# Optimization experiments

Hardware: AMD Instinct MI355X
Metric: run time of the kernel (lower is better)

Reference implementation:

```python
import jax, jax.numpy as jnp
import numpy as np

FILTER_LENGTH = 1024
HOP_LENGTH = 512
CUTOFF = FILTER_LENGTH // 2 + 1  # 513
PAD = FILTER_LENGTH // 2


def _make_forward_basis():
    # Real/imag DFT basis, rows = [Re(0..cutoff-1); Im(0..cutoff-1)], cols = time taps
    fb = np.fft.fft(np.eye(FILTER_LENGTH))
    basis = np.vstack([np.real(fb[:CUTOFF, :]), np.imag(fb[:CUTOFF, :])]).astype(np.float32)
    # periodic ('fftbins') Hann window, win_length == filter_length so no centering pad
    n = np.arange(FILTER_LENGTH)
    window = (0.5 - 0.5 * np.cos(2.0 * np.pi * n / FILTER_LENGTH)).astype(np.float32)
    return jnp.asarray(basis * window[None, :])  # [1026, 1024]


def setup_inputs() -> dict:
    key = jax.random.key(0)
    input_data = jax.random.normal(key, (16, 1048576), dtype=jnp.float32)
    forward_basis = _make_forward_basis()
    return {"input_data": input_data, "forward_basis": forward_basis}


def reference(input_data, forward_basis):
    # reflect-pad, frame, windowed DFT via conv1d, then magnitude
    x = jnp.pad(input_data, ((0, 0), (PAD, PAD)), mode="reflect")[:, None, :]  # [B,1,L+1024]
    y = jax.lax.conv_general_dilated(
        x,
        forward_basis[:, None, :],  # [1026, 1, 1024]
        window_strides=(HOP_LENGTH,),
        padding="VALID",
        dimension_numbers=("NCH", "OIH", "NCH"),
    )  # [B, 1026, T]
    real = y[:, :CUTOFF, :]
    imag = y[:, CUTOFF:, :]
    return jnp.sqrt(real * real + imag * imag)  # [B, 513, T]
```

## Files before the change

### kernel.cpp

```cpp
#include <hip/hip_runtime.h>
#include <math.h>

#define L_IN   1048576
#define NBATCH 16
#define T_FR   2049
#define NBINS  513

struct C2 { float r, i; };
__device__ __forceinline__ C2 cadd(C2 a, C2 b){ return {a.r+b.r, a.i+b.i}; }
__device__ __forceinline__ C2 csub(C2 a, C2 b){ return {a.r-b.r, a.i-b.i}; }
__device__ __forceinline__ C2 cmul(C2 a, C2 b){ return {a.r*b.r - a.i*b.i, a.r*b.i + a.i*b.r}; }
__device__ __forceinline__ C2 cnegi(C2 a){ return {a.i, -a.r}; }
#define RSQ2 0.70710678118654752f
__device__ __forceinline__ C2 cw8 (C2 a){ return { RSQ2*(a.r+a.i),  RSQ2*(a.i-a.r)}; }
__device__ __forceinline__ C2 cw83(C2 a){ return { RSQ2*(a.i-a.r), -RSQ2*(a.r+a.i)}; }

__device__ __forceinline__ void dft8(const C2 x[8], C2 y[8]) {
  C2 ea0 = cadd(x[0], x[4]), ea1 = csub(x[0], x[4]);
  C2 eb0 = cadd(x[2], x[6]), eb1 = csub(x[2], x[6]);
  C2 oa0 = cadd(x[1], x[5]), oa1 = csub(x[1], x[5]);
  C2 ob0 = cadd(x[3], x[7]), ob1 = csub(x[3], x[7]);
  C2 E0 = cadd(ea0, eb0), E2 = csub(ea0, eb0);
  C2 nb = cnegi(eb1);
  C2 E1 = cadd(ea1, nb),  E3 = csub(ea1, nb);
  C2 O0 = cadd(oa0, ob0), O2 = csub(oa0, ob0);
  C2 no = cnegi(ob1);
  C2 O1 = cadd(oa1, no),  O3 = csub(oa1, no);
  y[0] = cadd(E0, O0);  y[4] = csub(E0, O0);
  C2 t1 = cw8(O1);      y[1] = cadd(E1, t1); y[5] = csub(E1, t1);
  C2 t2 = cnegi(O2);    y[2] = cadd(E2, t2); y[6] = csub(E2, t2);
  C2 t3 = cw83(O3);     y[3] = cadd(E3, t3); y[7] = csub(E3, t3);
}

__device__ __forceinline__ int phys(int idx) { return idx ^ ((idx >> 4) & 15); }

__device__ __forceinline__ unsigned short f2bf(float f) {
  unsigned int u = __builtin_bit_cast(unsigned int, f);
  u += 0x7FFFu + ((u >> 16) & 1u);
  return (unsigned short)(u >> 16);
}

#define FENCE do { asm volatile("s_waitcnt lgkmcnt(0)" ::: "memory"); \
                   __builtin_amdgcn_sched_barrier(0); } while (0)

#define TWOPI 6.283185307179586f

__device__ __forceinline__ void load_raw(float2 v[8], const float* __restrict__ xb,
                                         int tt, int t) {
  const int s0 = tt*512 - 512;
  if (tt != 0 && tt != 2048) {
    #pragma unroll
    for (int j = 0; j < 8; ++j) v[j] = *(const float2*)&xb[s0 + 2*(t + 64*j)];
  } else {
    #pragma unroll
    for (int j = 0; j < 8; ++j) {
      int e0 = s0 + 2*(t + 64*j), e1 = e0 + 1;
      int r0 = e0 < 0 ? -e0 : (e0 >= L_IN ? 2*L_IN - 2 - e0 : e0);
      int r1 = e1 < 0 ? -e1 : (e1 >= L_IN ? 2*L_IN - 2 - e1 : e1);
      v[j] = { xb[r0], xb[r1] };
    }
  }
}

__device__ __forceinline__ void process_frame(const float2 v[8], const float2 wl[8],
    const C2 tws1[8], const C2 tws2[8], const C2 twu[8],
    C2* __restrict__ cfw, unsigned short (* __restrict__ mag)[18], int t, int tl)
{
  C2 x[8], y[8];
  #pragma unroll
  for (int j = 0; j < 8; ++j) x[j] = { v[j].x * wl[j].x, v[j].y * wl[j].y };
  dft8(x, y);
  #pragma unroll
  for (int k = 0; k < 8; ++k) cfw[phys(8*t + k)] = y[k];
  FENCE;
  {
    const int m = t & 7, g = t >> 3;
    C2 xs[8];
    #pragma unroll
    for (int j = 0; j < 8; ++j) xs[j] = cfw[phys(t + 64*j)];
    #pragma unroll
    for (int j = 1; j < 8; ++j) xs[j] = cmul(xs[j], tws1[j]);
    dft8(xs, y);
    #pragma unroll
    for (int k = 0; k < 8; ++k) cfw[phys(g*64 + m + 8*k)] = y[k];
  }
  FENCE;
  C2 z[8];
  {
    C2 xs[8];
    #pragma unroll
    for (int j = 0; j < 8; ++j) xs[j] = cfw[phys(t + 64*j)];
    FENCE;
    #pragma unroll
    for (int j = 1; j < 8; ++j) xs[j] = cmul(xs[j], tws2[j]);
    dft8(xs, z);
  }
  const int pl = (64 - t) & 63;
  #pragma unroll
  for (int j = 0; j < 8; ++j) {
    const int k = t + 64*j;
    C2 Zp = { __shfl(z[7-j].r, pl), __shfl(z[7-j].i, pl) };
    if (t == 0) Zp = z[(8-j) & 7];
    C2 Zk = z[j];
    C2 W  = twu[j];
    float Are = 0.5f*(Zk.r + Zp.r), Aim = 0.5f*(Zk.i - Zp.i);
    float Bre = 0.5f*(Zk.r - Zp.r), Bim = 0.5f*(Zk.i + Zp.i);
    float Xr = Are + (W.r*Bim + W.i*Bre);
    float Xi = Aim - (W.r*Bre - W.i*Bim);
    mag[k][tl] = f2bf(sqrtf(Xr*Xr + Xi*Xi));
  }
  if (t == 0) mag[512][tl] = f2bf(fabsf(z[0].r - z[0].i));
}

__global__ __launch_bounds__(256, 3)
void stft_fft(const float* __restrict__ input,
              const float* __restrict__ basis,
              float* __restrict__ out)
{
  __shared__ C2 cf[4][512];
  __shared__ unsigned short mag[513][18];

  const int tid = threadIdx.x;
  const int t   = tid & 63;
  const int w   = tid >> 6;
  const int b   = blockIdx.y;
  const int t0  = blockIdx.x << 4;

  C2 tws1[8], tws2[8], twu[8];
  {
    const int m = t & 7;
    #pragma unroll
    for (int j = 1; j < 8; ++j) {
      float s, c, a1 = (TWOPI/64.0f)  * (float)(m*j);
      __sincosf(a1, &s, &c); tws1[j] = { c, -s };
      float a2 = (TWOPI/512.0f) * (float)(t*j);
      __sincosf(a2, &s, &c); tws2[j] = { c, -s };
    }
    #pragma unroll
    for (int j = 0; j < 8; ++j) {
      float s, c, a = (TWOPI/1024.0f) * (float)(t + 64*j);
      __sincosf(a, &s, &c); twu[j] = { c, -s };
    }
  }

  float2 wl[8];
  #pragma unroll
  for (int j = 0; j < 8; ++j) wl[j] = *(const float2*)&basis[2*(t + 64*j)];

  const float* xb = input + (size_t)b * L_IN;
  C2* cfw = cf[w];
  const int base = t0 + w*4;

  float2 v0[8], v1[8];
  if (base     <= 2048) load_raw(v0, xb, base,     t);
  if (base + 1 <= 2048) load_raw(v1, xb, base + 1, t);
  if (base     <= 2048) process_frame(v0, wl, tws1, tws2, twu, cfw, mag, t, w*4);
  if (base + 2 <= 2048) load_raw(v0, xb, base + 2, t);
  if (base + 1 <= 2048) process_frame(v1, wl, tws1, tws2, twu, cfw, mag, t, w*4 + 1);
  if (base + 3 <= 2048) load_raw(v1, xb, base + 3, t);
  if (base + 2 <= 2048) process_frame(v0, wl, tws1, tws2, twu, cfw, mag, t, w*4 + 2);
  if (base + 3 <= 2048) process_frame(v1, wl, tws1, tws2, twu, cfw, mag, t, w*4 + 3);

  __syncthreads();

  const size_t ob = (size_t)b * NBINS * T_FR;
  for (int idx = tid; idx < NBINS*16; idx += 256) {
    const int row = idx >> 4, tl = idx & 15, tt = t0 + tl;
    if (tt <= 2048) {
      unsigned int u = (unsigned int)mag[row][tl] << 16;
      out[ob + (size_t)row * T_FR + tt] = __builtin_bit_cast(float, u);
    }
  }
}

extern "C" void kernel_launch(void* const* d_in, const int* in_sizes, int n_in,
                              void* d_out, int out_size, void* d_ws, size_t ws_size,
                              hipStream_t stream) {
  const float* input = (const float*)d_in[0];
  const float* basis = (const float*)d_in[1];
  float* out = (float*)d_out;
  stft_fft<<<dim3(129, 16), 256, 0, stream>>>(input, basis, out);
}
```

Baseline: 54.74 us.

## Process 32 frames per block, remap blocks across XCDs, drop LDS fences

Each block now handles 32 frames instead of 16, with each wave running 8 frames through a double-buffered load/process pipeline. Tail frames are clamped to the last valid frame rather than branched around. The grid becomes 1D and block IDs are swizzled so that neighbouring tiles of the same batch land on the same XCD. The explicit lgkmcnt waits and sched barriers between FFT stages are removed so the compiler can schedule LDS traffic itself. The goals are wider, better-coalesced output row stores, less per-block setup overhead, and more freedom for instruction scheduling. The cost is more LDS for the magnitude tile and redundant work on clamped tail frames.

```diff
diff --git a/kernel.cpp b/kernel.cpp
--- a/kernel.cpp
+++ b/kernel.cpp
@@ -40,9 +40,6 @@
   return (unsigned short)(u >> 16);
 }
 
-#define FENCE do { asm volatile("s_waitcnt lgkmcnt(0)" ::: "memory"); \
-                   __builtin_amdgcn_sched_barrier(0); } while (0)
-
 #define TWOPI 6.283185307179586f
 
 __device__ __forceinline__ void load_raw(float2 v[8], const float* __restrict__ xb,
@@ -64,7 +61,7 @@
 
 __device__ __forceinline__ void process_frame(const float2 v[8], const float2 wl[8],
     const C2 tws1[8], const C2 tws2[8], const C2 twu[8],
-    C2* __restrict__ cfw, unsigned short (* __restrict__ mag)[18], int t, int tl)
+    C2* __restrict__ cfw, unsigned short (* __restrict__ mag)[34], int t, int tl)
 {
   C2 x[8], y[8];
   #pragma unroll
@@ -72,7 +69,6 @@
   dft8(x, y);
   #pragma unroll
   for (int k = 0; k < 8; ++k) cfw[phys(8*t + k)] = y[k];
-  FENCE;
   {
     const int m = t & 7, g = t >> 3;
     C2 xs[8];
@@ -84,13 +80,11 @@
     #pragma unroll
     for (int k = 0; k < 8; ++k) cfw[phys(g*64 + m + 8*k)] = y[k];
   }
-  FENCE;
   C2 z[8];
   {
     C2 xs[8];
     #pragma unroll
     for (int j = 0; j < 8; ++j) xs[j] = cfw[phys(t + 64*j)];
-    FENCE;
     #pragma unroll
     for (int j = 1; j < 8; ++j) xs[j] = cmul(xs[j], tws2[j]);
     dft8(xs, z);
@@ -118,13 +112,16 @@
               float* __restrict__ out)
 {
   __shared__ C2 cf[4][512];
-  __shared__ unsigned short mag[513][18];
+  __shared__ unsigned short mag[513][34];
 
   const int tid = threadIdx.x;
   const int t   = tid & 63;
   const int w   = tid >> 6;
-  const int b   = blockIdx.y;
-  const int t0  = blockIdx.x << 4;
+
+  const int bid  = blockIdx.x;
+  const int wg   = (bid & 7) * 130 + (bid >> 3);
+  const int b    = wg / 65;
+  const int t0   = (wg - b * 65) << 5;
 
   C2 tws1[8], tws2[8], twu[8];
   {
@@ -149,23 +146,33 @@
 
   const float* xb = input + (size_t)b * L_IN;
   C2* cfw = cf[w];
-  const int base = t0 + w*4;
+  const int base = t0 + w*8;
+  const int f0 = base     < 2048 ? base     : 2048;
+  const int f1 = base + 1 < 2048 ? base + 1 : 2048;
+  const int f2 = base + 2 < 2048 ? base + 2 : 2048;
+  const int f3 = base + 3 < 2048 ? base + 3 : 2048;
+  const int f4 = base + 4 < 2048 ? base + 4 : 2048;
+  const int f5 = base + 5 < 2048 ? base + 5 : 2048;
+  const int f6 = base + 6 < 2048 ? base + 6 : 2048;
+  const int f7 = base + 7 < 2048 ? base + 7 : 2048;
 
-  float2 v0[8], v1[8];
-  if (base     <= 2048) load_raw(v0, xb, base,     t);
-  if (base + 1 <= 2048) load_raw(v1, xb, base + 1, t);
-  if (base     <= 2048) process_frame(v0, wl, tws1, tws2, twu, cfw, mag, t, w*4);
-  if (base + 2 <= 2048) load_raw(v0, xb, base + 2, t);
-  if (base + 1 <= 2048) process_frame(v1, wl, tws1, tws2, twu, cfw, mag, t, w*4 + 1);
-  if (base + 3 <= 2048) load_raw(v1, xb, base + 3, t);
-  if (base + 2 <= 2048) process_frame(v0, wl, tws1, tws2, twu, cfw, mag, t, w*4 + 2);
-  if (base + 3 <= 2048) process_frame(v1, wl, tws1, tws2, twu, cfw, mag, t, w*4 + 3);
+  float2 va[8], vb[8];
+  load_raw(va, xb, f0, t);
+  load_raw(vb, xb, f1, t);
+  process_frame(va, wl, tws1, tws2, twu, cfw, mag, t, w*8    ); load_raw(va, xb, f2, t);
+  process_frame(vb, wl, tws1, tws2, twu, cfw, mag, t, w*8 + 1); load_raw(vb, xb, f3, t);
+  process_frame(va, wl, tws1, tws2, twu, cfw, mag, t, w*8 + 2); load_raw(va, xb, f4, t);
+  process_frame(vb, wl, tws1, tws2, twu, cfw, mag, t, w*8 + 3); load_raw(vb, xb, f5, t);
+  process_frame(va, wl, tws1, tws2, twu, cfw, mag, t, w*8 + 4); load_raw(va, xb, f6, t);
+  process_frame(vb, wl, tws1, tws2, twu, cfw, mag, t, w*8 + 5); load_raw(vb, xb, f7, t);
+  process_frame(va, wl, tws1, tws2, twu, cfw, mag, t, w*8 + 6);
+  process_frame(vb, wl, tws1, tws2, twu, cfw, mag, t, w*8 + 7);
 
   __syncthreads();
 
   const size_t ob = (size_t)b * NBINS * T_FR;
-  for (int idx = tid; idx < NBINS*16; idx += 256) {
-    const int row = idx >> 4, tl = idx & 15, tt = t0 + tl;
+  for (int idx = tid; idx < NBINS*32; idx += 256) {
+    const int row = idx >> 5, tl = idx & 31, tt = t0 + tl;
     if (tt <= 2048) {
       unsigned int u = (unsigned int)mag[row][tl] << 16;
       out[ob + (size_t)row * T_FR + tt] = __builtin_bit_cast(float, u);
@@ -179,5 +186,5 @@
   const float* input = (const float*)d_in[0];
   const float* basis = (const float*)d_in[1];
   float* out = (float*)d_out;
-  stft_fft<<<dim3(129, 16), 256, 0, stream>>>(input, basis, out);
+  stft_fft<<<dim3(65 * 16), 256, 0, stream>>>(input, basis, out);
 }
```

Result: slower. 56.63 us (+3.4%).

## Use single-wavefront blocks processing eight frames each and drop LDS fences

Applied to the files above, without the earlier changes.

The kernel moves from 256-thread blocks, where four wavefronts each handle four frames, to 64-thread blocks where one wavefront handles eight frames with double-buffered loads. Out-of-range tail frames are clamped to frame 2048, so they are recomputed instead of skipped. Because each block is now a single wavefront, the explicit s_waitcnt/sched_barrier fences and the __syncthreads are removed, relying on in-order LDS access within a wave. The per-block LDS footprint shrinks and the block count doubles. In exchange, each output row write covers only 8 contiguous floats instead of 16, which weakens write coalescing.

```diff
diff --git a/kernel.cpp b/kernel.cpp
--- a/kernel.cpp
+++ b/kernel.cpp
@@ -40,9 +40,6 @@
   return (unsigned short)(u >> 16);
 }
 
-#define FENCE do { asm volatile("s_waitcnt lgkmcnt(0)" ::: "memory"); \
-                   __builtin_amdgcn_sched_barrier(0); } while (0)
-
 #define TWOPI 6.283185307179586f
 
 __device__ __forceinline__ void load_raw(float2 v[8], const float* __restrict__ xb,
@@ -64,7 +61,7 @@
 
 __device__ __forceinline__ void process_frame(const float2 v[8], const float2 wl[8],
     const C2 tws1[8], const C2 tws2[8], const C2 twu[8],
-    C2* __restrict__ cfw, unsigned short (* __restrict__ mag)[18], int t, int tl)
+    C2* __restrict__ cfw, unsigned short (* __restrict__ mag)[9], int t, int tl)
 {
   C2 x[8], y[8];
   #pragma unroll
@@ -72,7 +69,6 @@
   dft8(x, y);
   #pragma unroll
   for (int k = 0; k < 8; ++k) cfw[phys(8*t + k)] = y[k];
-  FENCE;
   {
     const int m = t & 7, g = t >> 3;
     C2 xs[8];
@@ -84,13 +80,11 @@
     #pragma unroll
     for (int k = 0; k < 8; ++k) cfw[phys(g*64 + m + 8*k)] = y[k];
   }
-  FENCE;
   C2 z[8];
   {
     C2 xs[8];
     #pragma unroll
     for (int j = 0; j < 8; ++j) xs[j] = cfw[phys(t + 64*j)];
-    FENCE;
     #pragma unroll
     for (int j = 1; j < 8; ++j) xs[j] = cmul(xs[j], tws2[j]);
     dft8(xs, z);
@@ -112,19 +106,17 @@
   if (t == 0) mag[512][tl] = f2bf(fabsf(z[0].r - z[0].i));
 }
 
-__global__ __launch_bounds__(256, 3)
+__global__ __launch_bounds__(64, 8)
 void stft_fft(const float* __restrict__ input,
               const float* __restrict__ basis,
               float* __restrict__ out)
 {
-  __shared__ C2 cf[4][512];
-  __shared__ unsigned short mag[513][18];
+  __shared__ C2 cf[512];
+  __shared__ unsigned short mag[513][9];
 
-  const int tid = threadIdx.x;
-  const int t   = tid & 63;
-  const int w   = tid >> 6;
-  const int b   = blockIdx.y;
-  const int t0  = blockIdx.x << 4;
+  const int t  = threadIdx.x;
+  const int b  = blockIdx.y;
+  const int t0 = blockIdx.x << 3;
 
   C2 tws1[8], tws2[8], twu[8];
   {
@@ -148,24 +140,31 @@
   for (int j = 0; j < 8; ++j) wl[j] = *(const float2*)&basis[2*(t + 64*j)];
 
   const float* xb = input + (size_t)b * L_IN;
-  C2* cfw = cf[w];
-  const int base = t0 + w*4;
+  const int f0 = t0     < 2048 ? t0     : 2048;
+  const int f1 = t0 + 1 < 2048 ? t0 + 1 : 2048;
+  const int f2 = t0 + 2 < 2048 ? t0 + 2 : 2048;
+  const int f3 = t0 + 3 < 2048 ? t0 + 3 : 2048;
+  const int f4 = t0 + 4 < 2048 ? t0 + 4 : 2048;
+  const int f5 = t0 + 5 < 2048 ? t0 + 5 : 2048;
+  const int f6 = t0 + 6 < 2048 ? t0 + 6 : 2048;
+  const int f7 = t0 + 7 < 2048 ? t0 + 7 : 2048;
 
-  float2 v0[8], v1[8];
-  if (base     <= 2048) load_raw(v0, xb, base,     t);
-  if (base + 1 <= 2048) load_raw(v1, xb, base + 1, t);
-  if (base     <= 2048) process_frame(v0, wl, tws1, tws2, twu, cfw, mag, t, w*4);
-  if (base + 2 <= 2048) load_raw(v0, xb, base + 2, t);
-  if (base + 1 <= 2048) process_frame(v1, wl, tws1, tws2, twu, cfw, mag, t, w*4 + 1);
-  if (base + 3 <= 2048) load_raw(v1, xb, base + 3, t);
-  if (base + 2 <= 2048) process_frame(v0, wl, tws1, tws2, twu, cfw, mag, t, w*4 + 2);
-  if (base + 3 <= 2048) process_frame(v1, wl, tws1, tws2, twu, cfw, mag, t, w*4 + 3);
+  float2 va[8], vb[8];
+  load_raw(va, xb, f0, t);
+  load_raw(vb, xb, f1, t);
+  process_frame(va, wl, tws1, tws2, twu, cf, mag, t, 0); load_raw(va, xb, f2, t);
+  process_frame(vb, wl, tws1, tws2, twu, cf, mag, t, 1); load_raw(vb, xb, f3, t);
+  process_frame(va, wl, tws1, tws2, twu, cf, mag, t, 2); load_raw(va, xb, f4, t);
+  process_frame(vb, wl, tws1, tws2, twu, cf, mag, t, 3); load_raw(vb, xb, f5, t);
+  process_frame(va, wl, tws1, tws2, twu, cf, mag, t, 4); load_raw(va, xb, f6, t);
+  process_frame(vb, wl, tws1, tws2, twu, cf, mag, t, 5); load_raw(vb, xb, f7, t);
+  process_frame(va, wl, tws1, tws2, twu, cf, mag, t, 6);
+  process_frame(vb, wl, tws1, tws2, twu, cf, mag, t, 7);
 
-  __syncthreads();
 
   const size_t ob = (size_t)b * NBINS * T_FR;
-  for (int idx = tid; idx < NBINS*16; idx += 256) {
-    const int row = idx >> 4, tl = idx & 15, tt = t0 + tl;
+  for (int idx = t; idx < NBINS*8; idx += 64) {
+    const int row = idx >> 3, tl = idx & 7, tt = t0 + tl;
     if (tt <= 2048) {
       unsigned int u = (unsigned int)mag[row][tl] << 16;
       out[ob + (size_t)row * T_FR + tt] = __builtin_bit_cast(float, u);
@@ -179,5 +178,5 @@
   const float* input = (const float*)d_in[0];
   const float* basis = (const float*)d_in[1];
   float* out = (float*)d_out;
-  stft_fft<<<dim3(129, 16), 256, 0, stream>>>(input, basis, out);
+  stft_fft<<<dim3(257, 16), 64, 0, stream>>>(input, basis, out);
 }
```

New measurement: 67.33 us. 1.23x slower.
